# Kernel optimization log

Measured on AMD Instinct MI355X. Metric: run time of the kernel, lower is better.

The kernel has to match this reference:

```python
import jax, jax.numpy as jnp
import numpy as np

NUM_HEADS = 12


def setup_inputs() -> dict:
    key = jax.random.key(0)
    ks = jax.random.split(key, 8)
    B, H, W, C = 1, 64, 64, 768
    hd = C // NUM_HEADS
    s = 0.02
    return {
        "hidden_states": jax.random.normal(ks[0], (B, H, W, C), jnp.float32),
        "q_w": jax.random.normal(ks[1], (C, C), jnp.float32) * s,
        "q_b": jnp.zeros((C,), jnp.float32),
        "k_w": jax.random.normal(ks[2], (C, C), jnp.float32) * s,
        "k_b": jnp.zeros((C,), jnp.float32),
        "v_w": jax.random.normal(ks[3], (C, C), jnp.float32) * s,
        "v_b": jnp.zeros((C,), jnp.float32),
        "proj_w": jax.random.normal(ks[4], (C, C), jnp.float32) * s,
        "proj_b": jnp.zeros((C,), jnp.float32),
        "rel_pos_h": jax.random.normal(ks[5], (2 * H - 1, hd), jnp.float32) * s,
        "rel_pos_w": jax.random.normal(ks[6], (2 * W - 1, hd), jnp.float32) * s,
    }


def reference(hidden_states, q_w, q_b, k_w, k_b, v_w, v_b, proj_w, proj_b,
              rel_pos_h, rel_pos_w):
    B, H, W, C = hidden_states.shape
    nh = NUM_HEADS
    hd = C // nh
    scale = hd ** -0.5

    x = hidden_states.reshape(B, H * W, C)

    def to_heads(t):  # [B, HW, C] -> [B*nh, HW, hd]
        return t.reshape(B, H * W, nh, hd).transpose(0, 2, 1, 3).reshape(B * nh, H * W, hd)

    q = to_heads(x @ q_w.T + q_b)
    k = to_heads(x @ k_w.T + k_b)
    v = to_heads(x @ v_w.T + v_b)

    # scaled QK^T: [B*nh, HW, HW]
    attn = jnp.einsum("bqd,bkd->bqk", q * scale, k)

    # decomposed relative position bias (q_size == k_size, so no interpolation)
    idx_h = jnp.arange(H)[:, None] - jnp.arange(H)[None, :] + (H - 1)
    idx_w = jnp.arange(W)[:, None] - jnp.arange(W)[None, :] + (W - 1)
    Rh = rel_pos_h[idx_h]  # [H, H, hd]
    Rw = rel_pos_w[idx_w]  # [W, W, hd]
    r_q = q.reshape(B * nh, H, W, hd)
    rel_h = jnp.einsum("bhwc,hkc->bhwk", r_q, Rh)  # [B*nh, H, W, H]
    rel_w = jnp.einsum("bhwc,wkc->bhwk", r_q, Rw)  # [B*nh, H, W, W]
    attn = (attn.reshape(B * nh, H, W, H, W)
            + rel_h[:, :, :, :, None]
            + rel_w[:, :, :, None, :]).reshape(B * nh, H * W, H * W)

    attn = jax.nn.softmax(attn.astype(jnp.float32), axis=-1).astype(q.dtype)
    # dropout p=0.0 in eval -> identity

    out = jnp.einsum("bqk,bkd->bqd", attn, v)
    out = out.reshape(B, nh, H, W, hd).transpose(0, 2, 3, 1, 4).reshape(B, H, W, C)
    out = out @ proj_w.T + proj_b
    return out
```

## Files before the change

### kernel.cpp

```cpp
#include <hip/hip_runtime.h>
#include <cstdint>
#include <cstddef>

#define T 4096
#define C 768
#define HD 64
#define NH 12

typedef float f32x4 __attribute__((ext_vector_type(4)));
typedef __bf16 bf16x8 __attribute__((ext_vector_type(8)));
typedef short s16x4 __attribute__((ext_vector_type(4)));
typedef unsigned short u16;

static __device__ __forceinline__ u16 f2bf(float f) {
    union { __bf16 h; u16 u; } cv;
    cv.h = (__bf16)f;
    return cv.u;
}

static __device__ __forceinline__ float exp2_hw(float x) {
    float r;
    asm("v_exp_f32 %0, %1" : "=v"(r) : "v"(x));
    return r;
}

static __device__ __forceinline__ void load_lds16(const void* g, void* l) {
    __builtin_amdgcn_global_load_lds(
        (const __attribute__((address_space(1))) void*)g,
        (__attribute__((address_space(3))) void*)l, 16, 0, 0);
}

static __device__ __forceinline__ void mfma16(f32x4& acc, s16x4 a, s16x4 b) {
#if defined(__HIP_DEVICE_COMPILE__)
#if __has_builtin(__builtin_amdgcn_mfma_f32_16x16x16bf16_1k)
    acc = __builtin_amdgcn_mfma_f32_16x16x16bf16_1k(a, b, acc, 0, 0, 0);
#else
    asm volatile("s_nop 2\n\t"
                 "v_mfma_f32_16x16x16_bf16 %0, %1, %2, %0\n\t"
                 "s_nop 7\n\t"
                 "s_nop 7"
                 : "+v"(acc) : "v"(a), "v"(b));
#endif
#else
    (void)acc; (void)a; (void)b;
#endif
}

__global__ __launch_bounds__(256) void cvt_all(
    const float* __restrict__ hs, const float* __restrict__ w0,
    const float* __restrict__ w1, const float* __restrict__ w2,
    const float* __restrict__ w3, const float* __restrict__ rh,
    const float* __restrict__ rw,
    u16* __restrict__ dhs, u16* __restrict__ dw0, u16* __restrict__ dw1,
    u16* __restrict__ dw2, u16* __restrict__ dw3, u16* __restrict__ drh,
    u16* __restrict__ drw) {
    const int NHS = T * C;
    const int NW = C * C;
    const int NR = 127 * HD;
    const int NTOT = NHS + 4 * NW + 2 * NR;
    int i = (blockIdx.x * 256 + threadIdx.x) * 4;
    if (i >= NTOT) return;
    const float* s; u16* d; int j;
    if (i < NHS) { s = hs; d = dhs; j = i; }
    else if (i < NHS + 4 * NW) {
        j = i - NHS;
        int t = j / NW; j -= t * NW;
        s = (t == 0) ? w0 : (t == 1) ? w1 : (t == 2) ? w2 : w3;
        d = (t == 0) ? dw0 : (t == 1) ? dw1 : (t == 2) ? dw2 : dw3;
    } else {
        j = i - NHS - 4 * NW;
        if (j < NR) { s = rh; d = drh; }
        else { s = rw; d = drw; j -= NR; }
    }
    float4 v = *(const float4*)(s + j);
    d[j + 0] = f2bf(v.x);
    d[j + 1] = f2bf(v.y);
    d[j + 2] = f2bf(v.z);
    d[j + 3] = f2bf(v.w);
}

__global__ __launch_bounds__(256, 2) void gemm_qkv_kernel(
    const u16* __restrict__ xb,
    const u16* __restrict__ wq, const u16* __restrict__ wk, const u16* __restrict__ wv,
    const float* __restrict__ qb, const float* __restrict__ kb, const float* __restrict__ vb,
    u16* __restrict__ Q, u16* __restrict__ K, u16* __restrict__ V) {
    __shared__ __align__(16) u16 As[2][128 * 64];
    __shared__ __align__(16) u16 Bs[2][128 * 64];
    const int z = blockIdx.z;
    const u16* W = (z == 0) ? wq : (z == 1) ? wk : wv;
    const float* bias = (z == 0) ? qb : (z == 1) ? kb : vb;
    u16* dst = (z == 0) ? Q : (z == 1) ? K : V;
    const int m0 = blockIdx.x * 128, n0 = blockIdx.y * 128;
    const int tid = threadIdx.x;
    const int wave = tid >> 6, lane = tid & 63, quad = lane >> 4, l15 = lane & 15;
    const int r0 = (wave >> 1) * 64, c0 = (wave & 1) * 64;
    int srow[4], sx[4], sdst[4];
#pragma unroll
    for (int i = 0; i < 4; ++i) {
        int p = i * 256 + wave * 64 + lane;
        srow[i] = p >> 3;
        sx[i] = (p & 7) ^ (srow[i] & 7);
        sdst[i] = (i * 256 + wave * 64) * 8;
    }
    f32x4 acc[4][4] = {};
#pragma unroll
    for (int i = 0; i < 4; ++i) {
        load_lds16(xb + (size_t)(m0 + srow[i]) * C + sx[i] * 8, &As[0][sdst[i]]);
        load_lds16(W + (size_t)(n0 + srow[i]) * C + sx[i] * 8, &Bs[0][sdst[i]]);
    }
    for (int kt = 0; kt < 12; ++kt) {
        const int cur = kt & 1;
        __syncthreads();
        if (kt < 11) {
            const int k0 = (kt + 1) * 64;
#pragma unroll
            for (int i = 0; i < 4; ++i) {
                load_lds16(xb + (size_t)(m0 + srow[i]) * C + k0 + sx[i] * 8, &As[cur ^ 1][sdst[i]]);
                load_lds16(W + (size_t)(n0 + srow[i]) * C + k0 + sx[i] * 8, &Bs[cur ^ 1][sdst[i]]);
            }
        }
#pragma unroll
        for (int kk = 0; kk < 2; ++kk) {
            bf16x8 af[4], bfr[4];
#pragma unroll
            for (int mi = 0; mi < 4; ++mi) {
                int r = r0 + mi * 16 + l15;
                af[mi] = *(const bf16x8*)&As[cur][r * 64 + (((kk * 4 + quad) ^ (r & 7)) * 8)];
            }
#pragma unroll
            for (int ni = 0; ni < 4; ++ni) {
                int r = c0 + ni * 16 + l15;
                bfr[ni] = *(const bf16x8*)&Bs[cur][r * 64 + (((kk * 4 + quad) ^ (r & 7)) * 8)];
            }
#pragma unroll
            for (int mi = 0; mi < 4; ++mi)
#pragma unroll
                for (int ni = 0; ni < 4; ++ni)
                    acc[mi][ni] = __builtin_amdgcn_mfma_f32_16x16x32_bf16(af[mi], bfr[ni], acc[mi][ni], 0, 0, 0);
        }
    }
#pragma unroll
    for (int mi = 0; mi < 4; ++mi)
#pragma unroll
        for (int ni = 0; ni < 4; ++ni)
#pragma unroll
            for (int r = 0; r < 4; ++r) {
                int m = m0 + r0 + mi * 16 + quad * 4 + r;
                int n = n0 + c0 + ni * 16 + l15;
                float v = acc[mi][ni][r] + bias[n];
                dst[(size_t)(n >> 6) * T * HD + (size_t)m * HD + (n & 63)] = f2bf(v);
            }
}

__global__ __launch_bounds__(256, 2) void gemm_proj_kernel(
    const u16* __restrict__ A, const u16* __restrict__ W,
    const float* __restrict__ bias, float* __restrict__ out) {
    __shared__ __align__(16) u16 As[2][128 * 64];
    __shared__ __align__(16) u16 Bs[2][128 * 64];
    const int m0 = blockIdx.x * 128, n0 = blockIdx.y * 128;
    const int tid = threadIdx.x;
    const int wave = tid >> 6, lane = tid & 63, quad = lane >> 4, l15 = lane & 15;
    const int r0 = (wave >> 1) * 64, c0 = (wave & 1) * 64;
    int srow[4], sx[4], sdst[4];
#pragma unroll
    for (int i = 0; i < 4; ++i) {
        int p = i * 256 + wave * 64 + lane;
        srow[i] = p >> 3;
        sx[i] = (p & 7) ^ (srow[i] & 7);
        sdst[i] = (i * 256 + wave * 64) * 8;
    }
    f32x4 acc[4][4] = {};
#pragma unroll
    for (int i = 0; i < 4; ++i) {
        load_lds16(A + (size_t)(m0 + srow[i]) * C + sx[i] * 8, &As[0][sdst[i]]);
        load_lds16(W + (size_t)(n0 + srow[i]) * C + sx[i] * 8, &Bs[0][sdst[i]]);
    }
    for (int kt = 0; kt < 12; ++kt) {
        const int cur = kt & 1;
        __syncthreads();
        if (kt < 11) {
            const int k0 = (kt + 1) * 64;
#pragma unroll
            for (int i = 0; i < 4; ++i) {
                load_lds16(A + (size_t)(m0 + srow[i]) * C + k0 + sx[i] * 8, &As[cur ^ 1][sdst[i]]);
                load_lds16(W + (size_t)(n0 + srow[i]) * C + k0 + sx[i] * 8, &Bs[cur ^ 1][sdst[i]]);
            }
        }
#pragma unroll
        for (int kk = 0; kk < 2; ++kk) {
            bf16x8 af[4], bfr[4];
#pragma unroll
            for (int mi = 0; mi < 4; ++mi) {
                int r = r0 + mi * 16 + l15;
                af[mi] = *(const bf16x8*)&As[cur][r * 64 + (((kk * 4 + quad) ^ (r & 7)) * 8)];
            }
#pragma unroll
            for (int ni = 0; ni < 4; ++ni) {
                int r = c0 + ni * 16 + l15;
                bfr[ni] = *(const bf16x8*)&Bs[cur][r * 64 + (((kk * 4 + quad) ^ (r & 7)) * 8)];
            }
#pragma unroll
            for (int mi = 0; mi < 4; ++mi)
#pragma unroll
                for (int ni = 0; ni < 4; ++ni)
                    acc[mi][ni] = __builtin_amdgcn_mfma_f32_16x16x32_bf16(af[mi], bfr[ni], acc[mi][ni], 0, 0, 0);
        }
    }
#pragma unroll
    for (int mi = 0; mi < 4; ++mi)
#pragma unroll
        for (int ni = 0; ni < 4; ++ni)
#pragma unroll
            for (int r = 0; r < 4; ++r) {
                int m = m0 + r0 + mi * 16 + quad * 4 + r;
                int n = n0 + c0 + ni * 16 + l15;
                out[(size_t)m * C + n] = acc[mi][ni][r] + bias[n];
            }
}

__global__ __launch_bounds__(256) void vtrans_kernel(const u16* __restrict__ V,
                                                     u16* __restrict__ Vt) {
    __shared__ __align__(16) u16 tl[64 * 72];
    const int h = blockIdx.y, t0 = blockIdx.x * 64, tid = threadIdx.x;
#pragma unroll
    for (int i = 0; i < 2; ++i) {
        int c = i * 256 + tid;
        int row = c >> 3, col = (c & 7) * 8;
        union { float4 f; u16 u[8]; } cv;
        cv.f = *(const float4*)(V + (size_t)h * T * HD + (size_t)(t0 + row) * HD + col);
#pragma unroll
        for (int j = 0; j < 8; ++j) tl[(col + j) * 72 + row] = cv.u[j];
    }
    __syncthreads();
#pragma unroll
    for (int i = 0; i < 2; ++i) {
        int c = i * 256 + tid;
        int drow = c >> 3, tcol = (c & 7) * 8;
        float4 v = *(const float4*)&tl[drow * 72 + tcol];
        *(float4*)(Vt + (size_t)(h * HD + drow) * T + t0 + tcol) = v;
    }
}

__global__ __launch_bounds__(256) void relh_kernel(const u16* __restrict__ Q,
                                                   const u16* __restrict__ rph,
                                                   float* __restrict__ relH) {
    const float LOG2E = 1.4426950408889634f;
    const int hq = blockIdx.x, h = blockIdx.y;
    const int tid = threadIdx.x, wave = tid >> 6, lane = tid & 63;
    const int quad = lane >> 4, l15 = lane & 15;
    f32x4 acc[4] = {};
    bf16x8 a[2], b[4][2];
#pragma unroll
    for (int kk = 0; kk < 2; ++kk) {
        int hk = wave * 16 + l15;
        a[kk] = *(const bf16x8*)(rph + (size_t)(hq - hk + 63) * HD + kk * 32 + quad * 8);
    }
#pragma unroll
    for (int nt = 0; nt < 4; ++nt)
#pragma unroll
        for (int kk = 0; kk < 2; ++kk)
            b[nt][kk] = *(const bf16x8*)(Q + (size_t)h * T * HD +
                                         (size_t)(hq * 64 + nt * 16 + l15) * HD + kk * 32 + quad * 8);
#pragma unroll
    for (int nt = 0; nt < 4; ++nt) {
        acc[nt] = __builtin_amdgcn_mfma_f32_16x16x32_bf16(a[0], b[nt][0], acc[nt], 0, 0, 0);
        acc[nt] = __builtin_amdgcn_mfma_f32_16x16x32_bf16(a[1], b[nt][1], acc[nt], 0, 0, 0);
    }
#pragma unroll
    for (int nt = 0; nt < 4; ++nt) {
        float4 v;
        v.x = acc[nt][0] * LOG2E; v.y = acc[nt][1] * LOG2E;
        v.z = acc[nt][2] * LOG2E; v.w = acc[nt][3] * LOG2E;
        *(float4*)(relH + (((size_t)(h * 64 + hq) * 64 + nt * 16 + l15) * 64) +
                   wave * 16 + quad * 4) = v;
    }
}

__global__ __launch_bounds__(256) void relw_kernel(const u16* __restrict__ Q,
                                                   const u16* __restrict__ rpw,
                                                   float* __restrict__ relW) {
    const float LOG2E = 1.4426950408889634f;
    const int wq = blockIdx.x, h = blockIdx.y;
    const int tid = threadIdx.x, wave = tid >> 6, lane = tid & 63;
    const int quad = lane >> 4, l15 = lane & 15;
    f32x4 acc[4] = {};
    bf16x8 a[2], b[4][2];
#pragma unroll
    for (int kk = 0; kk < 2; ++kk) {
        int hqr = wave * 16 + l15;
        a[kk] = *(const bf16x8*)(Q + (size_t)h * T * HD +
                                 (size_t)(hqr * 64 + wq) * HD + kk * 32 + quad * 8);
    }
#pragma unroll
    for (int nt = 0; nt < 4; ++nt)
#pragma unroll
        for (int kk = 0; kk < 2; ++kk) {
            int wk = nt * 16 + l15;
            b[nt][kk] = *(const bf16x8*)(rpw + (size_t)(wq - wk + 63) * HD + kk * 32 + quad * 8);
        }
#pragma unroll
    for (int nt = 0; nt < 4; ++nt) {
        acc[nt] = __builtin_amdgcn_mfma_f32_16x16x32_bf16(a[0], b[nt][0], acc[nt], 0, 0, 0);
        acc[nt] = __builtin_amdgcn_mfma_f32_16x16x32_bf16(a[1], b[nt][1], acc[nt], 0, 0, 0);
    }
#pragma unroll
    for (int nt = 0; nt < 4; ++nt)
#pragma unroll
        for (int r = 0; r < 4; ++r) {
            int hqr = wave * 16 + quad * 4 + r;
            relW[((size_t)h * T + hqr * 64 + wq) * 64 + nt * 16 + l15] = acc[nt][r] * LOG2E;
        }
}

__global__ __launch_bounds__(256, 3) void attn_kernel(
    const u16* __restrict__ Q, const u16* __restrict__ K, const u16* __restrict__ Vt,
    const float* __restrict__ relH, const float* __restrict__ relW,
    u16* __restrict__ AO) {
    __shared__ __align__(16) unsigned char smem[32768];
    u16* kb = (u16*)smem;
    u16* vb = (u16*)(smem + 16384);
    float* fs = (float*)smem;
    float* rs = (float*)(smem + 17408);

    const int hq = blockIdx.x, h = blockIdx.y;
    const int t0 = hq * 64;
    const int tid = threadIdx.x, w = tid >> 6, lane = tid & 63;
    const int quad = lane >> 4, l15 = lane & 15;
    const int qh = w >> 1, kh = w & 1;
    const float C1 = 0.18033688011112042f;

    const u16* Kbase = K + (size_t)h * T * HD;
    const u16* Vbase = Vt + (size_t)h * HD * T;

    const int p0 = w * 128 + lane, p1 = p0 + 64;
    const int sr0 = p0 >> 3, sx0 = (p0 & 7) ^ (sr0 & 7);
    const int sr1 = p1 >> 3, sx1 = (p1 & 7) ^ (sr1 & 7);
    const int lds0 = w * 1024, lds1 = w * 1024 + 512;

    bf16x8 qa[2][2];
#pragma unroll
    for (int b = 0; b < 2; ++b)
#pragma unroll
        for (int kk = 0; kk < 2; ++kk)
            qa[b][kk] = *(const bf16x8*)(Q + (size_t)h * T * HD +
                                         (size_t)(t0 + qh * 32 + b * 16 + l15) * HD + kk * 32 + quad * 8);
    f32x4 rw4[2][2];
#pragma unroll
    for (int b = 0; b < 2; ++b)
#pragma unroll
        for (int ks = 0; ks < 2; ++ks)
            rw4[b][ks] = *(const f32x4*)(relW + ((size_t)h * T + t0 + qh * 32 + b * 16 + l15) * 64 +
                                         kh * 32 + ks * 16 + quad * 4);
    const float* rhB = relH + ((size_t)(h * 64 + hq) * 64 + qh * 32 + l15) * 64;

    f32x4 oa[2][4] = {};
    float lsum[2] = {0.f, 0.f};

    load_lds16(Kbase + sr0 * HD + sx0 * 8, &kb[lds0]);
    load_lds16(Kbase + sr1 * HD + sx1 * 8, &kb[lds1]);
    load_lds16(Vbase + (size_t)sr0 * T + sx0 * 8, &vb[lds0]);
    load_lds16(Vbase + (size_t)sr1 * T + sx1 * 8, &vb[lds1]);

    for (int hk4 = 0; hk4 < 16; ++hk4) {
        f32x4 rh4[2];
        rh4[0] = *(const f32x4*)(rhB + hk4 * 4);
        rh4[1] = *(const f32x4*)(rhB + 16 * 64 + hk4 * 4);
#pragma unroll
        for (int rr = 0; rr < 4; ++rr) {
            const int hk = hk4 * 4 + rr;
            const int cur = rr & 1;
            __syncthreads();
            if (hk < 63) {
                const int tk0 = (hk + 1) * 64;
                load_lds16(Kbase + (size_t)(tk0 + sr0) * HD + sx0 * 8, &kb[(cur ^ 1) * 4096 + lds0]);
                load_lds16(Kbase + (size_t)(tk0 + sr1) * HD + sx1 * 8, &kb[(cur ^ 1) * 4096 + lds1]);
                load_lds16(Vbase + (size_t)sr0 * T + tk0 + sx0 * 8, &vb[(cur ^ 1) * 4096 + lds0]);
                load_lds16(Vbase + (size_t)sr1 * T + tk0 + sx1 * 8, &vb[(cur ^ 1) * 4096 + lds1]);
            }
            const u16* kc = kb + cur * 4096;
            const u16* vc = vb + cur * 4096;
            bf16x8 af[2][2];
#pragma unroll
            for (int ks = 0; ks < 2; ++ks)
#pragma unroll
                for (int kk = 0; kk < 2; ++kk)
                    af[ks][kk] = *(const bf16x8*)&kc[(kh * 32 + ks * 16 + l15) * 64 +
                                                     (((kk * 4 + quad) ^ (l15 & 7)) * 8)];
            s16x4 vf[4][2];
#pragma unroll
            for (int dg = 0; dg < 4; ++dg)
#pragma unroll
                for (int ks = 0; ks < 2; ++ks)
                    vf[dg][ks] = *(const s16x4*)&vc[(dg * 16 + l15) * 64 +
                                                    (((kh * 4 + ks * 2 + (quad >> 1)) ^ (l15 & 7)) * 8) +
                                                    (quad & 1) * 4];
#pragma unroll
            for (int b = 0; b < 2; ++b) {
                const float rhc = rh4[b][rr];
#pragma unroll
                for (int ks = 0; ks < 2; ++ks) {
                    f32x4 s4 = {};
                    s4 = __builtin_amdgcn_mfma_f32_16x16x32_bf16(af[ks][0], qa[b][0], s4, 0, 0, 0);
                    s4 = __builtin_amdgcn_mfma_f32_16x16x32_bf16(af[ks][1], qa[b][1], s4, 0, 0, 0);
                    float e0 = exp2_hw(s4[0] * C1 + rhc + rw4[b][ks][0]);
                    float e1 = exp2_hw(s4[1] * C1 + rhc + rw4[b][ks][1]);
                    float e2 = exp2_hw(s4[2] * C1 + rhc + rw4[b][ks][2]);
                    float e3 = exp2_hw(s4[3] * C1 + rhc + rw4[b][ks][3]);
                    lsum[b] += (e0 + e1) + (e2 + e3);
                    s16x4 pB;
                    pB[0] = (short)f2bf(e0); pB[1] = (short)f2bf(e1);
                    pB[2] = (short)f2bf(e2); pB[3] = (short)f2bf(e3);
#pragma unroll
                    for (int dg = 0; dg < 4; ++dg)
                        mfma16(oa[b][dg], vf[dg][ks], pB);
                }
            }
        }
    }
    __syncthreads();
#pragma unroll
    for (int b = 0; b < 2; ++b) {
        lsum[b] += __shfl_xor(lsum[b], 16);
        lsum[b] += __shfl_xor(lsum[b], 32);
    }
    if (kh == 1) {
        if (quad == 0) {
            rs[qh * 32 + l15] = lsum[0];
            rs[qh * 32 + 16 + l15] = lsum[1];
        }
#pragma unroll
        for (int b = 0; b < 2; ++b)
#pragma unroll
            for (int dg = 0; dg < 4; ++dg)
                *(f32x4*)&fs[(size_t)(qh * 32 + b * 16 + l15) * 68 + dg * 16 + quad * 4] = oa[b][dg];
    }
    __syncthreads();
    if (kh == 0) {
#pragma unroll
        for (int b = 0; b < 2; ++b) {
            const int q = qh * 32 + b * 16 + l15;
            const float inv = 1.0f / (lsum[b] + rs[q]);
#pragma unroll
            for (int dg = 0; dg < 4; ++dg) {
                f32x4 t4 = *(const f32x4*)&fs[(size_t)q * 68 + dg * 16 + quad * 4];
                float o0 = (oa[b][dg][0] + t4[0]) * inv;
                float o1 = (oa[b][dg][1] + t4[1]) * inv;
                float o2 = (oa[b][dg][2] + t4[2]) * inv;
                float o3 = (oa[b][dg][3] + t4[3]) * inv;
                uint2 st;
                st.x = (unsigned)f2bf(o0) | ((unsigned)f2bf(o1) << 16);
                st.y = (unsigned)f2bf(o2) | ((unsigned)f2bf(o3) << 16);
                *(uint2*)(AO + (size_t)(t0 + q) * C + h * 64 + dg * 16 + quad * 4) = st;
            }
        }
    }
}

extern "C" void kernel_launch(void* const* d_in, const int* in_sizes, int n_in,
                              void* d_out, int out_size, void* d_ws, size_t ws_size,
                              hipStream_t stream) {
    (void)in_sizes; (void)n_in; (void)out_size; (void)ws_size;
    const float* hs  = (const float*)d_in[0];
    const float* q_w = (const float*)d_in[1];
    const float* q_b = (const float*)d_in[2];
    const float* k_w = (const float*)d_in[3];
    const float* k_b = (const float*)d_in[4];
    const float* v_w = (const float*)d_in[5];
    const float* v_b = (const float*)d_in[6];
    const float* p_w = (const float*)d_in[7];
    const float* p_b = (const float*)d_in[8];
    const float* rph = (const float*)d_in[9];
    const float* rpw = (const float*)d_in[10];

    char* ws = (char*)d_ws;
    size_t off = 0;
    auto alloc = [&](size_t bytes) {
        void* p = ws + off;
        off = (off + bytes + 255) & ~(size_t)255;
        return p;
    };
    u16* xb   = (u16*)alloc((size_t)T * C * 2);
    u16* wqb  = (u16*)alloc((size_t)C * C * 2);
    u16* wkb  = (u16*)alloc((size_t)C * C * 2);
    u16* wvb  = (u16*)alloc((size_t)C * C * 2);
    u16* wpb  = (u16*)alloc((size_t)C * C * 2);
    u16* rphb = (u16*)alloc((size_t)127 * HD * 2);
    u16* rpwb = (u16*)alloc((size_t)127 * HD * 2);
    u16* Qb   = (u16*)alloc((size_t)NH * T * HD * 2);
    u16* Kb   = (u16*)alloc((size_t)NH * T * HD * 2);
    u16* Vb   = (u16*)alloc((size_t)NH * T * HD * 2);
    u16* Vt   = (u16*)alloc((size_t)NH * T * HD * 2);
    float* relH = (float*)alloc((size_t)NH * T * 64 * 4);
    float* relW = (float*)alloc((size_t)NH * T * 64 * 4);
    u16* AO   = (u16*)alloc((size_t)T * C * 2);

    const int NTOT = T * C + 4 * C * C + 2 * 127 * HD;
    cvt_all<<<dim3((NTOT / 4 + 255) / 256), dim3(256), 0, stream>>>(
        hs, q_w, k_w, v_w, p_w, rph, rpw, xb, wqb, wkb, wvb, wpb, rphb, rpwb);

    gemm_qkv_kernel<<<dim3(32, 6, 3), dim3(256), 0, stream>>>(
        xb, wqb, wkb, wvb, q_b, k_b, v_b, Qb, Kb, Vb);
    vtrans_kernel<<<dim3(64, NH), dim3(256), 0, stream>>>(Vb, Vt);
    relh_kernel<<<dim3(64, NH), dim3(256), 0, stream>>>(Qb, rphb, relH);
    relw_kernel<<<dim3(64, NH), dim3(256), 0, stream>>>(Qb, rpwb, relW);
    attn_kernel<<<dim3(64, NH), dim3(256), 0, stream>>>(Qb, Kb, Vt, relH, relW, AO);
    gemm_proj_kernel<<<dim3(32, 6), dim3(256), 0, stream>>>(AO, wpb, p_b, (float*)d_out);
}
```

Baseline: 233.9 us.

## Fuse V transpose into QKV epilogue, merge rel kernels, retile proj, MFMA rowsum

The QKV GEMM now writes V straight into transposed layout with packed 4-element stores, which removes the separate vtrans kernel and the intermediate V buffer. The relH and relW kernels become one launch selected by blockIdx.z. The projection GEMM drops to a 128x64 tile so it launches twice as many blocks. In attention, the softmax row sum is accumulated with an MFMA against a ones vector instead of scalar adds plus shuffles, adding one MFMA per step but freeing VALU work.

```diff
diff --git a/kernel.cpp b/kernel.cpp
--- a/kernel.cpp
+++ b/kernel.cpp
@@ -83,13 +83,13 @@
     const u16* __restrict__ xb,
     const u16* __restrict__ wq, const u16* __restrict__ wk, const u16* __restrict__ wv,
     const float* __restrict__ qb, const float* __restrict__ kb, const float* __restrict__ vb,
-    u16* __restrict__ Q, u16* __restrict__ K, u16* __restrict__ V) {
+    u16* __restrict__ Q, u16* __restrict__ K, u16* __restrict__ Vt) {
     __shared__ __align__(16) u16 As[2][128 * 64];
     __shared__ __align__(16) u16 Bs[2][128 * 64];
     const int z = blockIdx.z;
     const u16* W = (z == 0) ? wq : (z == 1) ? wk : wv;
     const float* bias = (z == 0) ? qb : (z == 1) ? kb : vb;
-    u16* dst = (z == 0) ? Q : (z == 1) ? K : V;
+    u16* dst = (z == 0) ? Q : (z == 1) ? K : Vt;
     const int m0 = blockIdx.x * 128, n0 = blockIdx.y * 128;
     const int tid = threadIdx.x;
     const int wave = tid >> 6, lane = tid & 63, quad = lane >> 4, l15 = lane & 15;
@@ -139,77 +139,101 @@
                     acc[mi][ni] = __builtin_amdgcn_mfma_f32_16x16x32_bf16(af[mi], bfr[ni], acc[mi][ni], 0, 0, 0);
         }
     }
-#pragma unroll
-    for (int mi = 0; mi < 4; ++mi)
-#pragma unroll
-        for (int ni = 0; ni < 4; ++ni)
-#pragma unroll
-            for (int r = 0; r < 4; ++r) {
-                int m = m0 + r0 + mi * 16 + quad * 4 + r;
+    if (z == 2) {
+#pragma unroll
+        for (int mi = 0; mi < 4; ++mi)
+#pragma unroll
+            for (int ni = 0; ni < 4; ++ni) {
+                int m = m0 + r0 + mi * 16 + quad * 4;
                 int n = n0 + c0 + ni * 16 + l15;
-                float v = acc[mi][ni][r] + bias[n];
-                dst[(size_t)(n >> 6) * T * HD + (size_t)m * HD + (n & 63)] = f2bf(v);
-            }
+                float b = bias[n];
+                uint2 st;
+                st.x = (unsigned)f2bf(acc[mi][ni][0] + b) |
+                       ((unsigned)f2bf(acc[mi][ni][1] + b) << 16);
+                st.y = (unsigned)f2bf(acc[mi][ni][2] + b) |
+                       ((unsigned)f2bf(acc[mi][ni][3] + b) << 16);
+                *(uint2*)(dst + (size_t)n * T + m) = st;
+            }
+    } else {
+#pragma unroll
+        for (int mi = 0; mi < 4; ++mi)
+#pragma unroll
+            for (int ni = 0; ni < 4; ++ni)
+#pragma unroll
+                for (int r = 0; r < 4; ++r) {
+                    int m = m0 + r0 + mi * 16 + quad * 4 + r;
+                    int n = n0 + c0 + ni * 16 + l15;
+                    float v = acc[mi][ni][r] + bias[n];
+                    dst[(size_t)(n >> 6) * T * HD + (size_t)m * HD + (n & 63)] = f2bf(v);
+                }
+    }
 }
 
 __global__ __launch_bounds__(256, 2) void gemm_proj_kernel(
     const u16* __restrict__ A, const u16* __restrict__ W,
     const float* __restrict__ bias, float* __restrict__ out) {
     __shared__ __align__(16) u16 As[2][128 * 64];
-    __shared__ __align__(16) u16 Bs[2][128 * 64];
-    const int m0 = blockIdx.x * 128, n0 = blockIdx.y * 128;
+    __shared__ __align__(16) u16 Bs[2][64 * 64];
+    const int m0 = blockIdx.x * 128, n0 = blockIdx.y * 64;
     const int tid = threadIdx.x;
     const int wave = tid >> 6, lane = tid & 63, quad = lane >> 4, l15 = lane & 15;
-    const int r0 = (wave >> 1) * 64, c0 = (wave & 1) * 64;
-    int srow[4], sx[4], sdst[4];
+    const int r0 = (wave >> 1) * 64, c0 = (wave & 1) * 32;
+    int srA[4], sxA[4], sdA[4], srB[2], sxB[2], sdB[2];
 #pragma unroll
     for (int i = 0; i < 4; ++i) {
         int p = i * 256 + wave * 64 + lane;
-        srow[i] = p >> 3;
-        sx[i] = (p & 7) ^ (srow[i] & 7);
-        sdst[i] = (i * 256 + wave * 64) * 8;
-    }
-    f32x4 acc[4][4] = {};
-#pragma unroll
-    for (int i = 0; i < 4; ++i) {
-        load_lds16(A + (size_t)(m0 + srow[i]) * C + sx[i] * 8, &As[0][sdst[i]]);
-        load_lds16(W + (size_t)(n0 + srow[i]) * C + sx[i] * 8, &Bs[0][sdst[i]]);
-    }
+        srA[i] = p >> 3; sxA[i] = (p & 7) ^ (srA[i] & 7);
+        sdA[i] = (i * 256 + wave * 64) * 8;
+    }
+#pragma unroll
+    for (int i = 0; i < 2; ++i) {
+        int p = i * 256 + wave * 64 + lane;
+        srB[i] = p >> 3; sxB[i] = (p & 7) ^ (srB[i] & 7);
+        sdB[i] = (i * 256 + wave * 64) * 8;
+    }
+    f32x4 acc[4][2] = {};
+#pragma unroll
+    for (int i = 0; i < 4; ++i)
+        load_lds16(A + (size_t)(m0 + srA[i]) * C + sxA[i] * 8, &As[0][sdA[i]]);
+#pragma unroll
+    for (int i = 0; i < 2; ++i)
+        load_lds16(W + (size_t)(n0 + srB[i]) * C + sxB[i] * 8, &Bs[0][sdB[i]]);
     for (int kt = 0; kt < 12; ++kt) {
         const int cur = kt & 1;
         __syncthreads();
         if (kt < 11) {
             const int k0 = (kt + 1) * 64;
 #pragma unroll
-            for (int i = 0; i < 4; ++i) {
-                load_lds16(A + (size_t)(m0 + srow[i]) * C + k0 + sx[i] * 8, &As[cur ^ 1][sdst[i]]);
-                load_lds16(W + (size_t)(n0 + srow[i]) * C + k0 + sx[i] * 8, &Bs[cur ^ 1][sdst[i]]);
-            }
+            for (int i = 0; i < 4; ++i)
+                load_lds16(A + (size_t)(m0 + srA[i]) * C + k0 + sxA[i] * 8, &As[cur ^ 1][sdA[i]]);
+#pragma unroll
+            for (int i = 0; i < 2; ++i)
+                load_lds16(W + (size_t)(n0 + srB[i]) * C + k0 + sxB[i] * 8, &Bs[cur ^ 1][sdB[i]]);
         }
 #pragma unroll
         for (int kk = 0; kk < 2; ++kk) {
-            bf16x8 af[4], bfr[4];
+            bf16x8 af[4], bfr[2];
 #pragma unroll
             for (int mi = 0; mi < 4; ++mi) {
                 int r = r0 + mi * 16 + l15;
                 af[mi] = *(const bf16x8*)&As[cur][r * 64 + (((kk * 4 + quad) ^ (r & 7)) * 8)];
             }
 #pragma unroll
-            for (int ni = 0; ni < 4; ++ni) {
+            for (int ni = 0; ni < 2; ++ni) {
                 int r = c0 + ni * 16 + l15;
                 bfr[ni] = *(const bf16x8*)&Bs[cur][r * 64 + (((kk * 4 + quad) ^ (r & 7)) * 8)];
             }
 #pragma unroll
             for (int mi = 0; mi < 4; ++mi)
 #pragma unroll
-                for (int ni = 0; ni < 4; ++ni)
+                for (int ni = 0; ni < 2; ++ni)
                     acc[mi][ni] = __builtin_amdgcn_mfma_f32_16x16x32_bf16(af[mi], bfr[ni], acc[mi][ni], 0, 0, 0);
         }
     }
 #pragma unroll
     for (int mi = 0; mi < 4; ++mi)
 #pragma unroll
-        for (int ni = 0; ni < 4; ++ni)
+        for (int ni = 0; ni < 2; ++ni)
 #pragma unroll
             for (int r = 0; r < 4; ++r) {
                 int m = m0 + r0 + mi * 16 + quad * 4 + r;
@@ -218,98 +242,71 @@
             }
 }
 
-__global__ __launch_bounds__(256) void vtrans_kernel(const u16* __restrict__ V,
-                                                     u16* __restrict__ Vt) {
-    __shared__ __align__(16) u16 tl[64 * 72];
-    const int h = blockIdx.y, t0 = blockIdx.x * 64, tid = threadIdx.x;
-#pragma unroll
-    for (int i = 0; i < 2; ++i) {
-        int c = i * 256 + tid;
-        int row = c >> 3, col = (c & 7) * 8;
-        union { float4 f; u16 u[8]; } cv;
-        cv.f = *(const float4*)(V + (size_t)h * T * HD + (size_t)(t0 + row) * HD + col);
-#pragma unroll
-        for (int j = 0; j < 8; ++j) tl[(col + j) * 72 + row] = cv.u[j];
-    }
-    __syncthreads();
-#pragma unroll
-    for (int i = 0; i < 2; ++i) {
-        int c = i * 256 + tid;
-        int drow = c >> 3, tcol = (c & 7) * 8;
-        float4 v = *(const float4*)&tl[drow * 72 + tcol];
-        *(float4*)(Vt + (size_t)(h * HD + drow) * T + t0 + tcol) = v;
-    }
-}
-
-__global__ __launch_bounds__(256) void relh_kernel(const u16* __restrict__ Q,
-                                                   const u16* __restrict__ rph,
-                                                   float* __restrict__ relH) {
+__global__ __launch_bounds__(256) void relhw_kernel(const u16* __restrict__ Q,
+                                                    const u16* __restrict__ rph,
+                                                    const u16* __restrict__ rpw,
+                                                    float* __restrict__ relH,
+                                                    float* __restrict__ relW) {
     const float LOG2E = 1.4426950408889634f;
-    const int hq = blockIdx.x, h = blockIdx.y;
+    const int h = blockIdx.y;
     const int tid = threadIdx.x, wave = tid >> 6, lane = tid & 63;
     const int quad = lane >> 4, l15 = lane & 15;
     f32x4 acc[4] = {};
     bf16x8 a[2], b[4][2];
-#pragma unroll
-    for (int kk = 0; kk < 2; ++kk) {
-        int hk = wave * 16 + l15;
-        a[kk] = *(const bf16x8*)(rph + (size_t)(hq - hk + 63) * HD + kk * 32 + quad * 8);
-    }
-#pragma unroll
-    for (int nt = 0; nt < 4; ++nt)
-#pragma unroll
-        for (int kk = 0; kk < 2; ++kk)
-            b[nt][kk] = *(const bf16x8*)(Q + (size_t)h * T * HD +
-                                         (size_t)(hq * 64 + nt * 16 + l15) * HD + kk * 32 + quad * 8);
-#pragma unroll
-    for (int nt = 0; nt < 4; ++nt) {
-        acc[nt] = __builtin_amdgcn_mfma_f32_16x16x32_bf16(a[0], b[nt][0], acc[nt], 0, 0, 0);
-        acc[nt] = __builtin_amdgcn_mfma_f32_16x16x32_bf16(a[1], b[nt][1], acc[nt], 0, 0, 0);
-    }
-#pragma unroll
-    for (int nt = 0; nt < 4; ++nt) {
-        float4 v;
-        v.x = acc[nt][0] * LOG2E; v.y = acc[nt][1] * LOG2E;
-        v.z = acc[nt][2] * LOG2E; v.w = acc[nt][3] * LOG2E;
-        *(float4*)(relH + (((size_t)(h * 64 + hq) * 64 + nt * 16 + l15) * 64) +
-                   wave * 16 + quad * 4) = v;
-    }
-}
-
-__global__ __launch_bounds__(256) void relw_kernel(const u16* __restrict__ Q,
-                                                   const u16* __restrict__ rpw,
-                                                   float* __restrict__ relW) {
-    const float LOG2E = 1.4426950408889634f;
-    const int wq = blockIdx.x, h = blockIdx.y;
-    const int tid = threadIdx.x, wave = tid >> 6, lane = tid & 63;
-    const int quad = lane >> 4, l15 = lane & 15;
-    f32x4 acc[4] = {};
-    bf16x8 a[2], b[4][2];
-#pragma unroll
-    for (int kk = 0; kk < 2; ++kk) {
-        int hqr = wave * 16 + l15;
-        a[kk] = *(const bf16x8*)(Q + (size_t)h * T * HD +
-                                 (size_t)(hqr * 64 + wq) * HD + kk * 32 + quad * 8);
-    }
-#pragma unroll
-    for (int nt = 0; nt < 4; ++nt)
+    if (blockIdx.z == 0) {
+        const int hq = blockIdx.x;
 #pragma unroll
         for (int kk = 0; kk < 2; ++kk) {
-            int wk = nt * 16 + l15;
-            b[nt][kk] = *(const bf16x8*)(rpw + (size_t)(wq - wk + 63) * HD + kk * 32 + quad * 8);
-        }
-#pragma unroll
-    for (int nt = 0; nt < 4; ++nt) {
-        acc[nt] = __builtin_amdgcn_mfma_f32_16x16x32_bf16(a[0], b[nt][0], acc[nt], 0, 0, 0);
-        acc[nt] = __builtin_amdgcn_mfma_f32_16x16x32_bf16(a[1], b[nt][1], acc[nt], 0, 0, 0);
-    }
-#pragma unroll
-    for (int nt = 0; nt < 4; ++nt)
-#pragma unroll
-        for (int r = 0; r < 4; ++r) {
-            int hqr = wave * 16 + quad * 4 + r;
-            relW[((size_t)h * T + hqr * 64 + wq) * 64 + nt * 16 + l15] = acc[nt][r] * LOG2E;
-        }
+            int hk = wave * 16 + l15;
+            a[kk] = *(const bf16x8*)(rph + (size_t)(hq - hk + 63) * HD + kk * 32 + quad * 8);
+        }
+#pragma unroll
+        for (int nt = 0; nt < 4; ++nt)
+#pragma unroll
+            for (int kk = 0; kk < 2; ++kk)
+                b[nt][kk] = *(const bf16x8*)(Q + (size_t)h * T * HD +
+                                             (size_t)(hq * 64 + nt * 16 + l15) * HD + kk * 32 + quad * 8);
+#pragma unroll
+        for (int nt = 0; nt < 4; ++nt) {
+            acc[nt] = __builtin_amdgcn_mfma_f32_16x16x32_bf16(a[0], b[nt][0], acc[nt], 0, 0, 0);
+            acc[nt] = __builtin_amdgcn_mfma_f32_16x16x32_bf16(a[1], b[nt][1], acc[nt], 0, 0, 0);
+        }
+#pragma unroll
+        for (int nt = 0; nt < 4; ++nt) {
+            float4 v;
+            v.x = acc[nt][0] * LOG2E; v.y = acc[nt][1] * LOG2E;
+            v.z = acc[nt][2] * LOG2E; v.w = acc[nt][3] * LOG2E;
+            *(float4*)(relH + (((size_t)(h * 64 + hq) * 64 + nt * 16 + l15) * 64) +
+                       wave * 16 + quad * 4) = v;
+        }
+    } else {
+        const int wq = blockIdx.x;
+#pragma unroll
+        for (int kk = 0; kk < 2; ++kk) {
+            int hqr = wave * 16 + l15;
+            a[kk] = *(const bf16x8*)(Q + (size_t)h * T * HD +
+                                     (size_t)(hqr * 64 + wq) * HD + kk * 32 + quad * 8);
+        }
+#pragma unroll
+        for (int nt = 0; nt < 4; ++nt)
+#pragma unroll
+            for (int kk = 0; kk < 2; ++kk) {
+                int wk = nt * 16 + l15;
+                b[nt][kk] = *(const bf16x8*)(rpw + (size_t)(wq - wk + 63) * HD + kk * 32 + quad * 8);
+            }
+#pragma unroll
+        for (int nt = 0; nt < 4; ++nt) {
+            acc[nt] = __builtin_amdgcn_mfma_f32_16x16x32_bf16(a[0], b[nt][0], acc[nt], 0, 0, 0);
+            acc[nt] = __builtin_amdgcn_mfma_f32_16x16x32_bf16(a[1], b[nt][1], acc[nt], 0, 0, 0);
+        }
+#pragma unroll
+        for (int nt = 0; nt < 4; ++nt)
+#pragma unroll
+            for (int r = 0; r < 4; ++r) {
+                int hqr = wave * 16 + quad * 4 + r;
+                relW[((size_t)h * T + hqr * 64 + wq) * 64 + nt * 16 + l15] = acc[nt][r] * LOG2E;
+            }
+    }
 }
 
 __global__ __launch_bounds__(256, 3) void attn_kernel(
@@ -353,8 +350,12 @@
                                          kh * 32 + ks * 16 + quad * 4);
     const float* rhB = relH + ((size_t)(h * 64 + hq) * 64 + qh * 32 + l15) * 64;
 
+    s16x4 ones;
+#pragma unroll
+    for (int j = 0; j < 4; ++j) ones[j] = (short)0x3F80;
+
     f32x4 oa[2][4] = {};
-    float lsum[2] = {0.f, 0.f};
+    f32x4 lacc[2] = {};
 
     load_lds16(Kbase + sr0 * HD + sx0 * 8, &kb[lds0]);
     load_lds16(Kbase + sr1 * HD + sx1 * 8, &kb[lds1]);
@@ -406,10 +407,10 @@
                     float e1 = exp2_hw(s4[1] * C1 + rhc + rw4[b][ks][1]);
                     float e2 = exp2_hw(s4[2] * C1 + rhc + rw4[b][ks][2]);
                     float e3 = exp2_hw(s4[3] * C1 + rhc + rw4[b][ks][3]);
-                    lsum[b] += (e0 + e1) + (e2 + e3);
                     s16x4 pB;
                     pB[0] = (short)f2bf(e0); pB[1] = (short)f2bf(e1);
                     pB[2] = (short)f2bf(e2); pB[3] = (short)f2bf(e3);
+                    mfma16(lacc[b], ones, pB);
 #pragma unroll
                     for (int dg = 0; dg < 4; ++dg)
                         mfma16(oa[b][dg], vf[dg][ks], pB);
@@ -418,15 +419,10 @@
         }
     }
     __syncthreads();
-#pragma unroll
-    for (int b = 0; b < 2; ++b) {
-        lsum[b] += __shfl_xor(lsum[b], 16);
-        lsum[b] += __shfl_xor(lsum[b], 32);
-    }
     if (kh == 1) {
         if (quad == 0) {
-            rs[qh * 32 + l15] = lsum[0];
-            rs[qh * 32 + 16 + l15] = lsum[1];
+            rs[qh * 32 + l15] = lacc[0][0];
+            rs[qh * 32 + 16 + l15] = lacc[1][0];
         }
 #pragma unroll
         for (int b = 0; b < 2; ++b)
@@ -439,7 +435,7 @@
 #pragma unroll
         for (int b = 0; b < 2; ++b) {
             const int q = qh * 32 + b * 16 + l15;
-            const float inv = 1.0f / (lsum[b] + rs[q]);
+            const float inv = 1.0f / (lacc[b][0] + rs[q]);
 #pragma unroll
             for (int dg = 0; dg < 4; ++dg) {
                 f32x4 t4 = *(const f32x4*)&fs[(size_t)q * 68 + dg * 16 + quad * 4];
@@ -488,7 +484,6 @@
     u16* rpwb = (u16*)alloc((size_t)127 * HD * 2);
     u16* Qb   = (u16*)alloc((size_t)NH * T * HD * 2);
     u16* Kb   = (u16*)alloc((size_t)NH * T * HD * 2);
-    u16* Vb   = (u16*)alloc((size_t)NH * T * HD * 2);
     u16* Vt   = (u16*)alloc((size_t)NH * T * HD * 2);
     float* relH = (float*)alloc((size_t)NH * T * 64 * 4);
     float* relW = (float*)alloc((size_t)NH * T * 64 * 4);
@@ -499,10 +494,8 @@
         hs, q_w, k_w, v_w, p_w, rph, rpw, xb, wqb, wkb, wvb, wpb, rphb, rpwb);
 
     gemm_qkv_kernel<<<dim3(32, 6, 3), dim3(256), 0, stream>>>(
-        xb, wqb, wkb, wvb, q_b, k_b, v_b, Qb, Kb, Vb);
-    vtrans_kernel<<<dim3(64, NH), dim3(256), 0, stream>>>(Vb, Vt);
-    relh_kernel<<<dim3(64, NH), dim3(256), 0, stream>>>(Qb, rphb, relH);
-    relw_kernel<<<dim3(64, NH), dim3(256), 0, stream>>>(Qb, rpwb, relW);
+        xb, wqb, wkb, wvb, q_b, k_b, v_b, Qb, Kb, Vt);
+    relhw_kernel<<<dim3(64, NH, 2), dim3(256), 0, stream>>>(Qb, rphb, rpwb, relH, relW);
     attn_kernel<<<dim3(64, NH), dim3(256), 0, stream>>>(Qb, Kb, Vt, relH, relW, AO);
-    gemm_proj_kernel<<<dim3(32, 6), dim3(256), 0, stream>>>(AO, wpb, p_b, (float*)d_out);
-}
+    gemm_proj_kernel<<<dim3(32, 12), dim3(256), 0, stream>>>(AO, wpb, p_b, (float*)d_out);
+}
```

Result: faster. 222.9 us (-4.7%).
